# Kernel tuning notes

Hardware: AMD Instinct MI355X
Metric: run time of the kernel (lower is better)

## Reference

```python
import jax, jax.numpy as jnp
import numpy as np

N = 50000      # num nodes (genes)
E = 800000     # num edges (TF->Target)
IN = 128       # in_channels
HID = 16       # hidden_channels per head
HEADS = 4
OUT = 32       # out_channels
NEG_SLOPE = 0.2  # PyG GATConv leaky_relu slope
EPS = 1e-16


def setup_inputs() -> dict:
    key = jax.random.key(0)
    ks = jax.random.split(key, 11)
    x = jax.random.normal(ks[0], (N, IN), dtype=jnp.float32)
    edge_index = jax.random.randint(ks[1], (2, E), 0, N, dtype=jnp.int32)
    # layer 1: heads=HEADS, concat=True
    W1 = jax.random.normal(ks[2], (IN, HEADS * HID), dtype=jnp.float32) * (1.0 / np.sqrt(IN))
    a_src1 = jax.random.normal(ks[3], (HEADS, HID), dtype=jnp.float32) * 0.1
    a_dst1 = jax.random.normal(ks[4], (HEADS, HID), dtype=jnp.float32) * 0.1
    b1 = jnp.zeros((HEADS * HID,), dtype=jnp.float32)
    # layer 2: heads=1, concat=False
    W2 = jax.random.normal(ks[5], (HEADS * HID, OUT), dtype=jnp.float32) * (1.0 / np.sqrt(HEADS * HID))
    a_src2 = jax.random.normal(ks[6], (1, OUT), dtype=jnp.float32) * 0.1
    a_dst2 = jax.random.normal(ks[7], (1, OUT), dtype=jnp.float32) * 0.1
    b2 = jnp.zeros((OUT,), dtype=jnp.float32)
    return dict(x=x, edge_index=edge_index, W1=W1, a_src1=a_src1, a_dst1=a_dst1, b1=b1,
                W2=W2, a_src2=a_src2, a_dst2=a_dst2, b2=b2)


def gat_layer(x, edge_index, W, a_src, a_dst, b, concat):
    """PyG GATConv (no self-loops, eval mode): gather -> edge attention -> segment softmax -> scatter."""
    n = x.shape[0]
    heads, ch = a_src.shape
    h = (x @ W).reshape(n, heads, ch)                      # [N, H, C]
    alpha_s = jnp.einsum('nhc,hc->nh', h, a_src)           # [N, H]
    alpha_d = jnp.einsum('nhc,hc->nh', h, a_dst)           # [N, H]
    src, dst = edge_index[0], edge_index[1]
    e = jax.nn.leaky_relu(alpha_s[src] + alpha_d[dst], negative_slope=NEG_SLOPE)  # [E, H]
    # numerically stable softmax over incoming edges of each dst node
    m = jax.ops.segment_max(e, dst, num_segments=n)        # [N, H]
    e = jnp.exp(e - m[dst])
    denom = jax.ops.segment_sum(e, dst, num_segments=n)    # [N, H]
    alpha = e / (denom[dst] + EPS)                         # [E, H]
    msg = h[src] * alpha[:, :, None]                       # [E, H, C]
    out = jax.ops.segment_sum(msg, dst, num_segments=n)    # [N, H, C]
    if concat:
        out = out.reshape(n, heads * ch)
    else:
        out = out.mean(axis=1)
    return out + b


def reference(x, edge_index, W1, a_src1, a_dst1, b1, W2, a_src2, a_dst2, b2):
    h = gat_layer(x, edge_index, W1, a_src1, a_dst1, b1, concat=True)   # [N, HEADS*HID]
    h = jax.nn.elu(h)
    out = gat_layer(h, edge_index, W2, a_src2, a_dst2, b2, concat=False)  # [N, OUT]
    return out
```

## Files before the change

kernel.cpp:

```cpp
#include <hip/hip_runtime.h>
#include <hip/hip_fp16.h>
#include <math.h>

#define NN 50000
#define NE 800000
#define INCH 128
#define HID1 16
#define H1 4
#define C1 64
#define C2 32
#define NEG 0.2f
#define EPSF 1e-16f
#define CAP 128
#define BSH 7
#define NBKT 391
#define CAPB 3072
#define EPB 2048
#define NPB1 391
#define GB1 782
#define POISON 0xAAAAAAAAu

static __device__ __forceinline__ float lrelu(float v){ return v > 0.f ? v : NEG * v; }


__global__ __launch_bounds__(256) void k_part1(
        const int* __restrict__ ei, unsigned* bcnt, unsigned* __restrict__ pairs,
        const float* __restrict__ x, const float* __restrict__ W,
        const float* __restrict__ asrc, const float* __restrict__ adst,
        __half* __restrict__ h, float* __restrict__ as1, float* __restrict__ ad1){
    __shared__ __align__(16) char smem[41472];
    int t = threadIdx.x;

    if (blockIdx.x < NPB1){
        int* hist = (int*)smem;
        int* scn  = (int*)(smem + 2048);
        int* spos = (int*)(smem + 4096);
        unsigned* gbase = (unsigned*)(smem + 6144);
        unsigned* stg   = (unsigned*)(smem + 7708);
        hist[t] = 0; hist[t + 256] = 0;
        __syncthreads();

        int e0 = blockIdx.x * EPB;
        int tot = NE - e0; if (tot > EPB) tot = EPB;
        unsigned pk[8]; int rnk[8], bkt[8];
        #pragma unroll
        for (int k = 0; k < 8; ++k){
            int idx = k * 256 + t;
            if (idx < tot){
                int e = e0 + idx;
                int s = ei[e];
                int d = ei[NE + e];
                bkt[k] = d >> BSH;
                pk[k] = ((unsigned)bkt[k] << 23) | ((unsigned)(d & 127) << 16) | (unsigned)s;
                rnk[k] = atomicAdd(&hist[bkt[k]], 1);
            } else bkt[k] = -1;
        }
        __syncthreads();

        int* sA = hist; int* sB = scn;
        for (int off = 1; off < 512; off <<= 1){
            int v0 = sA[t]       + ((t       >= off) ? sA[t - off]       : 0);
            int v1 = sA[t + 256] + ((t + 256 >= off) ? sA[t + 256 - off] : 0);
            __syncthreads();
            sB[t] = v0; sB[t + 256] = v1;
            __syncthreads();
            int* tmp = sA; sA = sB; sB = tmp;
        }
        for (int b = t; b < NBKT; b += 256){
            int incl = sA[b];
            int excl = (b > 0) ? sA[b - 1] : 0;
            spos[b] = excl;
            int cnt = incl - excl;
            unsigned off = 0;
            if (cnt > 0){
                unsigned old = atomicAdd(&bcnt[b], (unsigned)cnt);
                off = old - POISON;
                if (off > (unsigned)(CAPB - cnt)) off = 0;
            }
            gbase[b] = off;
        }
        __syncthreads();

        #pragma unroll
        for (int k = 0; k < 8; ++k)
            if (bkt[k] >= 0)
                stg[spos[bkt[k]] + rnk[k]] = pk[k];
        __syncthreads();

        for (int i = t; i < tot; i += 256){
            unsigned v = stg[i];
            int b = v >> 23;
            pairs[b * CAPB + gbase[b] + (i - spos[b])] = v;
        }
    } else {
        float* WS = (float*)smem;
        float (*XTc)[68] = (float(*)[68])(smem + 32768);
        int bid = blockIdx.x - NPB1;

        const float4* W4 = (const float4*)W;
        float4* WS4 = (float4*)WS;
        #pragma unroll
        for (int i = 0; i < 8; ++i) WS4[i * 256 + t] = W4[i * 256 + t];

        int nodeL = t >> 2;
        int kc = t & 3;
        int g = bid * 64 + nodeL;
        int gc = min(g, NN - 1);
        const float4* xr = (const float4*)(x + (size_t)gc * INCH);

        int tx = t & 15, ty = t >> 4;
        int c4 = tx * 4, n4 = ty * 4;
        float acc[4][4];
        #pragma unroll
        for (int a = 0; a < 4; ++a)
            #pragma unroll
            for (int b2 = 0; b2 < 4; ++b2) acc[a][b2] = 0.f;

        for (int ch = 0; ch < 4; ++ch){
            __syncthreads();
            float4 v0 = xr[ch * 8 + kc * 2 + 0];
            float4 v1 = xr[ch * 8 + kc * 2 + 1];
            int kb = kc * 8;
            XTc[kb + 0][nodeL] = v0.x; XTc[kb + 1][nodeL] = v0.y;
            XTc[kb + 2][nodeL] = v0.z; XTc[kb + 3][nodeL] = v0.w;
            XTc[kb + 4][nodeL] = v1.x; XTc[kb + 5][nodeL] = v1.y;
            XTc[kb + 6][nodeL] = v1.z; XTc[kb + 7][nodeL] = v1.w;
            __syncthreads();
            const float* Wc = WS + ch * 32 * C1;
            #pragma unroll 8
            for (int k = 0; k < 32; ++k){
                float4 xa = *(const float4*)&XTc[k][n4];
                float4 wb = *(const float4*)&Wc[k * C1 + c4];
                const float xv[4] = {xa.x, xa.y, xa.z, xa.w};
                const float wv[4] = {wb.x, wb.y, wb.z, wb.w};
                #pragma unroll
                for (int a = 0; a < 4; ++a)
                    #pragma unroll
                    for (int b2 = 0; b2 < 4; ++b2)
                        acc[a][b2] = fmaf(xv[a], wv[b2], acc[a][b2]);
            }
        }

        int hd = tx >> 2;
        #pragma unroll
        for (int a = 0; a < 4; ++a){
            int n = bid * 64 + n4 + a;
            if (n < NN){
                union { __half2 q[2]; float2 f; } u;
                u.q[0] = __floats2half2_rn(acc[a][0], acc[a][1]);
                u.q[1] = __floats2half2_rn(acc[a][2], acc[a][3]);
                *(float2*)&h[n * C1 + c4] = u.f;
            }
            float sa = 0.f, da = 0.f;
            #pragma unroll
            for (int b2 = 0; b2 < 4; ++b2){
                sa = fmaf(acc[a][b2], asrc[hd * HID1 + (c4 & 15) + b2], sa);
                da = fmaf(acc[a][b2], adst[hd * HID1 + (c4 & 15) + b2], da);
            }
            sa += __shfl_xor(sa, 1); sa += __shfl_xor(sa, 2);
            da += __shfl_xor(da, 1); da += __shfl_xor(da, 2);
            if ((tx & 3) == 0 && n < NN){
                as1[n * H1 + hd] = sa;
                ad1[n * H1 + hd] = da;
            }
        }
    }
}


__global__ __launch_bounds__(256) void k_build2(
        const unsigned* __restrict__ pairs, const unsigned* __restrict__ bcnt,
        int* __restrict__ rows, int* __restrict__ deg, int* __restrict__ srcs){
    __shared__ __align__(16) char smem[13824];
    int t = threadIdx.x;

    unsigned* stg = (unsigned*)smem;
    int* hist = (int*)(smem + 12288);
    int* scn  = (int*)(smem + 12800);
    int* cur  = (int*)(smem + 13312);
    int b = blockIdx.x;
    int n0 = b << BSH;
    unsigned cntu = bcnt[b] - POISON;
    if (cntu > (unsigned)CAPB) cntu = (b == NBKT - 1) ? 0u : (unsigned)CAPB;
    int cnt = (int)cntu;
    if (t < 128) hist[t] = 0;
    __syncthreads();
    const unsigned* psrc = pairs + b * CAPB;
    for (int i = t; i < cnt; i += 256){
        unsigned v = psrc[i];
        stg[i] = v;
        atomicAdd(&hist[(v >> 16) & 127], 1);
    }
    __syncthreads();
    int v = (t < 128) ? hist[t] : 0;
    if (t < 128) scn[t] = v;
    __syncthreads();
    for (int off = 1; off < 128; off <<= 1){
        int add = (t < 128 && t >= off) ? scn[t - off] : 0;
        __syncthreads();
        if (t < 128) scn[t] += add;
        __syncthreads();
    }
    if (t < 128){
        int base = b * CAPB + (scn[t] - v);
        cur[t] = base;
        int n = n0 + t;
        if (n < NN){ rows[n] = base; deg[n] = v; }
    }
    __syncthreads();
    for (int i = t; i < cnt; i += 256){
        unsigned pv = stg[i];
        int p = atomicAdd(&cur[(pv >> 16) & 127], 1);
        srcs[p] = (int)(pv & 0xFFFFu);
    }
}


__global__ __launch_bounds__(256) void k_aggA(
        const int* __restrict__ srcs, const int* __restrict__ rows,
        const int* __restrict__ deg, const __half* __restrict__ h1,
        const float* __restrict__ as, const float* __restrict__ ad,
        const float* __restrict__ b1, float* __restrict__ hp){
    __shared__ float vbuf[4][H1][132];
    __shared__ int   sbuf[4][CAP];
    int t = threadIdx.x;
    int w = t >> 6, lane = t & 63;
    int hd1 = lane & 3, eb = lane >> 2;
    int node = blockIdx.x * 4 + w;
    int start = rows[node], dg = deg[node];

    if (dg <= CAP){
        int dgp = (dg + 15) & ~15;
        for (int j = lane; j < dgp; j += 64)
            sbuf[w][j] = (j < dg) ? srcs[start + j] : 0;

        int hd2 = lane >> 4;
        const __half* hc = h1 + lane;
        __half hv[16];
        #pragma unroll
        for (int k = 0; k < 16; ++k)
            hv[k] = hc[sbuf[w][k] * C1];

        float adv = ad[node * H1 + hd1];
        float ssum = 0.f;
        for (int j = eb; j < dg; j += 16){
            int s = sbuf[w][j];
            float wv = __expf(lrelu(as[s * H1 + hd1] + adv));
            vbuf[w][hd1][j] = wv;
            ssum += wv;
        }
        if (lane < dgp - dg){
            int j = dg + lane;
            vbuf[w][0][j] = 0.f; vbuf[w][1][j] = 0.f;
            vbuf[w][2][j] = 0.f; vbuf[w][3][j] = 0.f;
        }
        ssum += __shfl_xor(ssum, 4);
        ssum += __shfl_xor(ssum, 8);
        ssum += __shfl_xor(ssum, 16);
        ssum += __shfl_xor(ssum, 32);
        float inv = 1.f / (__shfl(ssum, hd2) + EPSF);

        const float* wrow = vbuf[w][hd2];
        float a0 = 0.f, a1 = 0.f, a2 = 0.f, a3 = 0.f;
        #pragma unroll
        for (int k = 0; k < 16; k += 4){
            a0 = fmaf(__half2float(hv[k + 0]), wrow[k + 0], a0);
            a1 = fmaf(__half2float(hv[k + 1]), wrow[k + 1], a1);
            a2 = fmaf(__half2float(hv[k + 2]), wrow[k + 2], a2);
            a3 = fmaf(__half2float(hv[k + 3]), wrow[k + 3], a3);
        }
        for (int j0 = 16; j0 < dgp; j0 += 16){
            #pragma unroll
            for (int k = 0; k < 16; ++k)
                hv[k] = hc[sbuf[w][j0 + k] * C1];
            #pragma unroll
            for (int k = 0; k < 16; k += 4){
                a0 = fmaf(__half2float(hv[k + 0]), wrow[j0 + k + 0], a0);
                a1 = fmaf(__half2float(hv[k + 1]), wrow[j0 + k + 1], a1);
                a2 = fmaf(__half2float(hv[k + 2]), wrow[j0 + k + 2], a2);
                a3 = fmaf(__half2float(hv[k + 3]), wrow[j0 + k + 3], a3);
            }
        }
        float o = ((a0 + a1) + (a2 + a3)) * inv + b1[lane];
        hp[(size_t)node * C1 + lane] = o > 0.f ? o : (__expf(o) - 1.f);
    } else {
        int hdf = lane >> 4;
        float adv = ad[node * H1 + hdf];
        float ss = 0.f, ac = 0.f;
        for (int j = 0; j < dg; ++j){
            int s = srcs[start + j];
            float wv = __expf(lrelu(as[s * H1 + hdf] + adv));
            ss += wv;
            ac = fmaf(__half2float(h1[s * C1 + lane]), wv, ac);
        }
        float o = ac / (ss + EPSF) + b1[lane];
        hp[(size_t)node * C1 + lane] = o > 0.f ? o : (__expf(o) - 1.f);
    }
}


__global__ __launch_bounds__(256) void k_h2(
        const float* __restrict__ hp, const float* __restrict__ W2,
        const float* __restrict__ a2s, const float* __restrict__ a2d,
        __half* __restrict__ h2, float* __restrict__ as2, float* __restrict__ ad2){
    __shared__ float W2s[C1 * C2];
    __shared__ float tile[128][66];
    int t = threadIdx.x;
    int n0 = blockIdx.x * 128;

    const float4* w4 = (const float4*)W2;
    float4* ws4 = (float4*)W2s;
    ws4[t] = w4[t];
    ws4[t + 256] = w4[t + 256];

    const float4* hp4 = (const float4*)hp;
    #pragma unroll
    for (int i = 0; i < 8; ++i){
        int idx = i * 256 + t;
        int r = idx >> 4;
        int c4 = (idx & 15) << 2;
        int gn = n0 + r; if (gn >= NN) gn = NN - 1;
        float4 v = hp4[(size_t)gn * 16 + (idx & 15)];
        tile[r][c4 + 0] = v.x; tile[r][c4 + 1] = v.y;
        tile[r][c4 + 2] = v.z; tile[r][c4 + 3] = v.w;
    }
    __syncthreads();

    int n = t >> 1, hf = t & 1;
    int gn = n0 + n;
    float acc[16];
    #pragma unroll
    for (int c = 0; c < 16; ++c) acc[c] = 0.f;
    #pragma unroll 4
    for (int k = 0; k < C1; ++k){
        float hv = tile[n][k];
        const float* wk = W2s + k * C2 + hf * 16;
        #pragma unroll
        for (int c = 0; c < 16; ++c) acc[c] = fmaf(hv, wk[c], acc[c]);
    }
    float sa = 0.f, da = 0.f;
    #pragma unroll
    for (int c = 0; c < 16; ++c){
        sa = fmaf(acc[c], a2s[hf * 16 + c], sa);
        da = fmaf(acc[c], a2d[hf * 16 + c], da);
    }
    sa += __shfl_xor(sa, 1);
    da += __shfl_xor(da, 1);
    if (gn < NN){
        union { __half2 q[8]; float4 f[2]; } u;
        #pragma unroll
        for (int c2 = 0; c2 < 8; ++c2)
            u.q[c2] = __floats2half2_rn(acc[2 * c2], acc[2 * c2 + 1]);
        *(float4*)&h2[(size_t)gn * C2 + hf * 16]     = u.f[0];
        *(float4*)&h2[(size_t)gn * C2 + hf * 16 + 8] = u.f[1];
        if (hf == 0){ as2[gn] = sa; ad2[gn] = da; }
    }
}


__global__ __launch_bounds__(256) void k_agg2(
        const int* __restrict__ srcs, const int* __restrict__ rows,
        const int* __restrict__ deg, const __half* __restrict__ h2,
        const float* __restrict__ as, const float* __restrict__ ad,
        const float* __restrict__ b2, float* __restrict__ out){
    __shared__ float vbuf[8][CAP];
    __shared__ int   sbuf[8][CAP];
    int sl = threadIdx.x >> 5;
    int lane = threadIdx.x & 31;
    int node = blockIdx.x * 8 + sl;
    int start = rows[node], dg = deg[node];
    float adv = ad[node];

    if (dg <= CAP){
        int dgp = (dg + 15) & ~15;
        for (int j = lane; j < dgp; j += 32)
            sbuf[sl][j] = (j < dg) ? srcs[start + j] : 0;

        const __half* hc = h2 + lane;
        __half hv[16];
        #pragma unroll
        for (int k = 0; k < 16; ++k)
            hv[k] = hc[sbuf[sl][k] * C2];

        float ssum = 0.f;
        for (int j = lane; j < dg; j += 32){
            int s = sbuf[sl][j];
            float wv = __expf(lrelu(as[s] + adv));
            vbuf[sl][j] = wv;
            ssum += wv;
        }
        if (lane < dgp - dg) vbuf[sl][dg + lane] = 0.f;
        #pragma unroll
        for (int off = 1; off < 32; off <<= 1) ssum += __shfl_xor(ssum, off);
        float inv = 1.f / (ssum + EPSF);

        const float* wrow = vbuf[sl];
        float a0 = 0.f, a1 = 0.f, a2 = 0.f, a3 = 0.f;
        #pragma unroll
        for (int k = 0; k < 16; k += 4){
            a0 = fmaf(__half2float(hv[k + 0]), wrow[k + 0], a0);
            a1 = fmaf(__half2float(hv[k + 1]), wrow[k + 1], a1);
            a2 = fmaf(__half2float(hv[k + 2]), wrow[k + 2], a2);
            a3 = fmaf(__half2float(hv[k + 3]), wrow[k + 3], a3);
        }
        for (int j0 = 16; j0 < dgp; j0 += 16){
            #pragma unroll
            for (int k = 0; k < 16; ++k)
                hv[k] = hc[sbuf[sl][j0 + k] * C2];
            #pragma unroll
            for (int k = 0; k < 16; k += 4){
                a0 = fmaf(__half2float(hv[k + 0]), wrow[j0 + k + 0], a0);
                a1 = fmaf(__half2float(hv[k + 1]), wrow[j0 + k + 1], a1);
                a2 = fmaf(__half2float(hv[k + 2]), wrow[j0 + k + 2], a2);
                a3 = fmaf(__half2float(hv[k + 3]), wrow[j0 + k + 3], a3);
            }
        }
        out[node * C2 + lane] = ((a0 + a1) + (a2 + a3)) * inv + b2[lane];
    } else {
        float ss = 0.f, ac = 0.f;
        for (int j = 0; j < dg; ++j){
            int s = srcs[start + j];
            float wv = __expf(lrelu(as[s] + adv));
            ss += wv;
            ac = fmaf(__half2float(h2[s * C2 + lane]), wv, ac);
        }
        out[node * C2 + lane] = ac / (ss + EPSF) + b2[lane];
    }
}

extern "C" void kernel_launch(void* const* d_in, const int* in_sizes, int n_in,
                              void* d_out, int out_size, void* d_ws, size_t ws_size,
                              hipStream_t stream) {
    const float* x    = (const float*)d_in[0];
    const int*   ei   = (const int*)  d_in[1];
    const float* W1   = (const float*)d_in[2];
    const float* as1w = (const float*)d_in[3];
    const float* ad1w = (const float*)d_in[4];
    const float* b1   = (const float*)d_in[5];
    const float* W2   = (const float*)d_in[6];
    const float* as2w = (const float*)d_in[7];
    const float* ad2w = (const float*)d_in[8];
    const float* b2   = (const float*)d_in[9];
    float* out = (float*)d_out;

    float* p = (float*)d_ws;
    __half* h1 = (__half*)p; p += (size_t)NN * C1 / 2;
    __half* h2 = (__half*)p; p += (size_t)NN * C2 / 2;
    float* hp  = p; p += (size_t)NN * C1;
    float* as1  = p; p += (size_t)NN * H1;
    float* ad1  = p; p += (size_t)NN * H1;
    float* as2  = p; p += NN;
    float* ad2  = p; p += NN;
    int* deg  = (int*)p; p += NN;
    int* rows = (int*)p; p += NN;
    unsigned* bcnt = (unsigned*)p; p += NBKT + 57;
    int* srcs = (int*)p; p += (size_t)NBKT * CAPB;
    unsigned* pairs = (unsigned*)p;

    dim3 B(256);
    k_part1 <<<NPB1 + GB1, B, 0, stream>>>(ei, bcnt, pairs,
                                           x, W1, as1w, ad1w, h1, as1, ad1);
    k_build2<<<NBKT, B, 0, stream>>>(pairs, bcnt, rows, deg, srcs);
    k_aggA  <<<NN / 4, B, 0, stream>>>(srcs, rows, deg, h1, as1, ad1, b1, hp);
    k_h2    <<<NBKT, B, 0, stream>>>(hp, W2, as2w, ad2w, h2, as2, ad2);
    k_agg2  <<<NN / 8, B, 0, stream>>>(srcs, rows, deg, h2, as2, ad2, b2, out);
}
```

Measured before the change: 170.6 us.

## Double-buffer x tiles in projection GEMM and use wave-shuffle bucket scan

The bucket-partition branch replaces a 9-step shared-memory Hillis-Steele scan over 512 counters, which had two barriers per step, with a per-wavefront shuffle scan plus a small cross-wave fixup. The GEMM branch double-buffers the transposed x chunk in shared memory, issuing the global load for the next chunk before computing the current one, so load latency overlaps compute and one barrier per chunk is dropped. Shared memory per block grows from about 41 KB to 50 KB, which can lower occupancy on the GEMM blocks.

```diff
diff --git a/kernel.cpp b/kernel.cpp
--- a/kernel.cpp
+++ b/kernel.cpp
@@ -28,7 +28,7 @@
         const float* __restrict__ x, const float* __restrict__ W,
         const float* __restrict__ asrc, const float* __restrict__ adst,
         __half* __restrict__ h, float* __restrict__ as1, float* __restrict__ ad1){
-    __shared__ __align__(16) char smem[41472];
+    __shared__ __align__(16) char smem[50176];
     int t = threadIdx.x;
 
     if (blockIdx.x < NPB1){
@@ -36,7 +36,8 @@
         int* scn  = (int*)(smem + 2048);
         int* spos = (int*)(smem + 4096);
         unsigned* gbase = (unsigned*)(smem + 6144);
-        unsigned* stg   = (unsigned*)(smem + 7708);
+        int* wtot = (int*)(smem + 7708);
+        unsigned* stg   = (unsigned*)(smem + 7724);
         hist[t] = 0; hist[t + 256] = 0;
         __syncthreads();
 
@@ -57,15 +58,28 @@
         }
         __syncthreads();
 
-        int* sA = hist; int* sB = scn;
-        for (int off = 1; off < 512; off <<= 1){
-            int v0 = sA[t]       + ((t       >= off) ? sA[t - off]       : 0);
-            int v1 = sA[t + 256] + ((t + 256 >= off) ? sA[t + 256 - off] : 0);
+        {
+            int wv = t >> 6, ln = t & 63;
+            int base = wv * 128 + ln * 2;
+            int a = hist[base], b = hist[base + 1];
+            int s = a + b;
+            #pragma unroll
+            for (int off = 1; off < 64; off <<= 1){
+                int u = __shfl_up(s, off);
+                if (ln >= off) s += u;
+            }
+            if (ln == 63) wtot[wv] = s;
+            int excl = s - (a + b);
             __syncthreads();
-            sB[t] = v0; sB[t + 256] = v1;
-            __syncthreads();
-            int* tmp = sA; sA = sB; sB = tmp;
-        }
+            int addp = 0;
+            #pragma unroll
+            for (int p = 0; p < 3; ++p) if (p < wv) addp += wtot[p];
+            scn[base]     = addp + excl + a;
+            scn[base + 1] = addp + excl + a + b;
+        }
+        __syncthreads();
+
+        int* sA = scn;
         for (int b = t; b < NBKT; b += 256){
             int incl = sA[b];
             int excl = (b > 0) ? sA[b - 1] : 0;
@@ -94,7 +108,8 @@
         }
     } else {
         float* WS = (float*)smem;
-        float (*XTc)[68] = (float(*)[68])(smem + 32768);
+        float (*XT0)[68] = (float(*)[68])(smem + 32768);
+        float (*XT1)[68] = (float(*)[68])(smem + 41472);
         int bid = blockIdx.x - NPB1;
 
         const float4* W4 = (const float4*)W;
@@ -108,6 +123,17 @@
         int gc = min(g, NN - 1);
         const float4* xr = (const float4*)(x + (size_t)gc * INCH);
 
+        {
+            float4 v0 = xr[kc * 2 + 0];
+            float4 v1 = xr[kc * 2 + 1];
+            int kb = kc * 8;
+            XT0[kb + 0][nodeL] = v0.x; XT0[kb + 1][nodeL] = v0.y;
+            XT0[kb + 2][nodeL] = v0.z; XT0[kb + 3][nodeL] = v0.w;
+            XT0[kb + 4][nodeL] = v1.x; XT0[kb + 5][nodeL] = v1.y;
+            XT0[kb + 6][nodeL] = v1.z; XT0[kb + 7][nodeL] = v1.w;
+        }
+        __syncthreads();
+
         int tx = t & 15, ty = t >> 4;
         int c4 = tx * 4, n4 = ty * 4;
         float acc[4][4];
@@ -117,15 +143,12 @@
             for (int b2 = 0; b2 < 4; ++b2) acc[a][b2] = 0.f;
 
         for (int ch = 0; ch < 4; ++ch){
-            __syncthreads();
-            float4 v0 = xr[ch * 8 + kc * 2 + 0];
-            float4 v1 = xr[ch * 8 + kc * 2 + 1];
-            int kb = kc * 8;
-            XTc[kb + 0][nodeL] = v0.x; XTc[kb + 1][nodeL] = v0.y;
-            XTc[kb + 2][nodeL] = v0.z; XTc[kb + 3][nodeL] = v0.w;
-            XTc[kb + 4][nodeL] = v1.x; XTc[kb + 5][nodeL] = v1.y;
-            XTc[kb + 6][nodeL] = v1.z; XTc[kb + 7][nodeL] = v1.w;
-            __syncthreads();
+            float4 n0_, n1_;
+            if (ch < 3){
+                n0_ = xr[(ch + 1) * 8 + kc * 2 + 0];
+                n1_ = xr[(ch + 1) * 8 + kc * 2 + 1];
+            }
+            const float (*XTc)[68] = (ch & 1) ? XT1 : XT0;
             const float* Wc = WS + ch * 32 * C1;
             #pragma unroll 8
             for (int k = 0; k < 32; ++k){
@@ -138,6 +161,15 @@
                     #pragma unroll
                     for (int b2 = 0; b2 < 4; ++b2)
                         acc[a][b2] = fmaf(xv[a], wv[b2], acc[a][b2]);
+            }
+            if (ch < 3){
+                float (*XTn)[68] = (ch & 1) ? XT0 : XT1;
+                int kb = kc * 8;
+                XTn[kb + 0][nodeL] = n0_.x; XTn[kb + 1][nodeL] = n0_.y;
+                XTn[kb + 2][nodeL] = n0_.z; XTn[kb + 3][nodeL] = n0_.w;
+                XTn[kb + 4][nodeL] = n1_.x; XTn[kb + 5][nodeL] = n1_.y;
+                XTn[kb + 6][nodeL] = n1_.z; XTn[kb + 7][nodeL] = n1_.w;
+                __syncthreads();
             }
         }
 
```

New measurement: 170.8 us (median of 2 runs). No clear change (+0.1%).
